# Optimization experiments

Hardware: AMD Instinct MI355X
Metric: run time of the kernel (lower is better)

Reference implementation:

```python
import jax, jax.numpy as jnp
import numpy as np

N, E, IN, H = 50000, 800000, 128, 64
BN_EPS = 1e-5


def _bn(x, g, b, m, v):
    return (x - m) * jax.lax.rsqrt(v + BN_EPS) * g + b


def _gat(x, src, dst, W, a_s, a_d, bias):
    # PyG GATConv (heads=1): project, per-edge attention with self-loops,
    # segment softmax over destination, scatter-weighted aggregation.
    h = x @ W                                  # [N, H]
    as_n = h @ a_s                             # [N]
    ad_n = h @ a_d                             # [N]
    e = jax.nn.leaky_relu(as_n[src] + ad_n[dst], 0.2)   # [E+N]
    emax = jax.ops.segment_max(e, dst, num_segments=N)
    ex = jnp.exp(e - emax[dst])
    denom = jax.ops.segment_sum(ex, dst, num_segments=N)
    alpha = ex / (denom[dst] + 1e-16)
    out = jax.ops.segment_sum(alpha[:, None] * h[src], dst, num_segments=N)
    return out + bias


def setup_inputs() -> dict:
    key = jax.random.key(0)
    ks = jax.random.split(key, 24)
    inp = {}
    inp['x'] = jax.random.normal(ks[0], (N, IN), dtype=jnp.float32)
    inp['edge_index'] = jax.random.randint(ks[1], (2, E), 0, N, dtype=jnp.int32)
    s = 0.1
    inp['conv1_W'] = jax.random.normal(ks[2], (IN, H)) * s
    inp['conv1_as'] = jax.random.normal(ks[3], (H,)) * s
    inp['conv1_ad'] = jax.random.normal(ks[4], (H,)) * s
    inp['conv1_b'] = jnp.zeros((H,))
    inp['convW'] = jax.random.normal(ks[5], (4, H, H)) * s
    inp['conv_as'] = jax.random.normal(ks[6], (4, H)) * s
    inp['conv_ad'] = jax.random.normal(ks[7], (4, H)) * s
    inp['conv_b'] = jnp.zeros((4, H))
    inp['bn_g'] = jnp.ones((5, H))
    inp['bn_b'] = jnp.zeros((5, H))
    inp['bn_m'] = jax.random.normal(ks[8], (5, H)) * 0.01
    inp['bn_v'] = jnp.ones((5, H))
    inp['projW'] = jax.random.normal(ks[9], (4, H, H)) * s
    inp['projb'] = jnp.zeros((4, H))
    inp['hW1'] = jax.random.normal(ks[10], (H, H // 2)) * s
    inp['hb1'] = jnp.zeros((H // 2,))
    inp['hbn_g'] = jnp.ones((H // 2,))
    inp['hbn_b'] = jnp.zeros((H // 2,))
    inp['hbn_m'] = jax.random.normal(ks[11], (H // 2,)) * 0.01
    inp['hbn_v'] = jnp.ones((H // 2,))
    inp['hW2'] = jax.random.normal(ks[12], (H // 2, 1)) * s
    inp['hb2'] = jnp.zeros((1,))
    return inp


def reference(x, edge_index, conv1_W, conv1_as, conv1_ad, conv1_b, convW, conv_as, conv_ad, conv_b, bn_g, bn_b, bn_m, bn_v, projW, projb, hW1, hb1, hbn_g, hbn_b, hbn_m, hbn_v, hW2, hb2):
    loop = jnp.arange(N, dtype=edge_index.dtype)
    src = jnp.concatenate([edge_index[0], loop])  # self-loops (PyG default)
    dst = jnp.concatenate([edge_index[1], loop])

    x1 = jax.nn.relu(_gat(x, src, dst, conv1_W, conv1_as, conv1_ad, conv1_b))
    x1 = _bn(x1, bn_g[0], bn_b[0], bn_m[0], bn_v[0])

    xp = x1
    for l in range(4):  # conv2..conv5 (dropout identity in eval)
        xc = jax.nn.relu(_gat(xp, src, dst, convW[l], conv_as[l], conv_ad[l], conv_b[l]))
        xc = _bn(xc, bn_g[l + 1], bn_b[l + 1], bn_m[l + 1], bn_v[l + 1]) + (xp @ projW[l] + projb[l])
        xp = xc

    g = jnp.mean(xp, axis=0, keepdims=True)      # global_mean_pool, single graph -> [1, H]
    h1 = jax.nn.relu(g @ hW1 + hb1)
    h1 = _bn(h1, hbn_g, hbn_b, hbn_m, hbn_v)
    out = (h1 @ hW2 + hb2).squeeze(-1)           # [1]
    return out
```

## Files before the change

kernel.cpp:

```cpp
#include <hip/hip_runtime.h>
#include <hip/hip_fp16.h>

#define N_NODES 50000
#define N_EDGES 800000
#define IN_F 128
#define H_F 64
#define BN_EPS 1e-5f
#define MAXDEG 48
#define POOL_NB 256

__device__ inline unsigned pkh2(float a, float b) {
    __half2 t = __floats2half2_rn(a, b);
    return *(unsigned*)&t;
}
__device__ inline float2 uph2(unsigned u) {
    __half2 t = *(__half2*)&u;
    return __half22float2(t);
}


__global__ void k_init(int* __restrict__ cnt, unsigned short* __restrict__ ssrc) {
    int i = blockIdx.x * 256 + threadIdx.x;
    if (i < N_NODES) { cnt[i] = 1; ssrc[(size_t)i * MAXDEG] = (unsigned short)i; }
}

__global__ void k_scatter(const int* __restrict__ src, const int* __restrict__ dst,
                          int* __restrict__ cnt, unsigned short* __restrict__ ssrc) {
    int i = blockIdx.x * 256 + threadIdx.x;
    int e = i * 4;
    if (e + 3 < N_EDGES) {
        int4 s4 = *(const int4*)(src + e);
        int4 d4 = *(const int4*)(dst + e);
        int p0 = atomicAdd(&cnt[d4.x], 1);
        if (p0 < MAXDEG) ssrc[(size_t)d4.x * MAXDEG + p0] = (unsigned short)s4.x;
        int p1 = atomicAdd(&cnt[d4.y], 1);
        if (p1 < MAXDEG) ssrc[(size_t)d4.y * MAXDEG + p1] = (unsigned short)s4.y;
        int p2 = atomicAdd(&cnt[d4.z], 1);
        if (p2 < MAXDEG) ssrc[(size_t)d4.z * MAXDEG + p2] = (unsigned short)s4.z;
        int p3 = atomicAdd(&cnt[d4.w], 1);
        if (p3 < MAXDEG) ssrc[(size_t)d4.w * MAXDEG + p3] = (unsigned short)s4.w;
    } else {
        for (int k = e; k < N_EDGES; k++) {
            int s = src[k], d = dst[k];
            int p = atomicAdd(&cnt[d], 1);
            if (p < MAXDEG) ssrc[(size_t)d * MAXDEG + p] = (unsigned short)s;
        }
    }
}

__global__ __launch_bounds__(256) void k_gemm1(
        const float* __restrict__ x, const float* __restrict__ W,
        const float* __restrict__ a_s, const float* __restrict__ a_d,
        __half* __restrict__ hh, float* __restrict__ asn, float* __restrict__ adn) {
    __shared__ float Xs[64 * 129];
    __shared__ float asb[4][64], adb[4][64];
    int t = threadIdx.x, lane = t & 63, wave = t >> 6;
    int row0 = blockIdx.x * 64;
    for (int i = t; i < 64 * IN_F; i += 256) {
        int r = i >> 7, c = i & 127;
        Xs[r * 129 + c] = (row0 + r < N_NODES) ? x[(size_t)(row0 + r) * IN_F + c] : 0.f;
    }
    __syncthreads();
    int jb = __builtin_amdgcn_readfirstlane(wave << 4);
    float acc[16];
    #pragma unroll
    for (int j = 0; j < 16; j++) acc[j] = 0.f;
    for (int k0 = 0; k0 < IN_F; k0 += 8) {
        float xr[8];
        #pragma unroll
        for (int kk = 0; kk < 8; kk++) xr[kk] = Xs[lane * 129 + k0 + kk];
        #pragma unroll
        for (int kk = 0; kk < 8; kk++) {
            const float* wr = W + (k0 + kk) * H_F + jb;
            #pragma unroll
            for (int j = 0; j < 16; j++) acc[j] = fmaf(xr[kk], wr[j], acc[j]);
        }
    }
    int row = row0 + lane;
    float pa = 0.f, pd = 0.f;
    #pragma unroll
    for (int j = 0; j < 16; j++) { pa += acc[j] * a_s[jb + j]; pd += acc[j] * a_d[jb + j]; }
    asb[wave][lane] = pa; adb[wave][lane] = pd;
    if (row < N_NODES) {
        uint4 w0, w1;
        w0.x = pkh2(acc[0],  acc[1]);  w0.y = pkh2(acc[2],  acc[3]);
        w0.z = pkh2(acc[4],  acc[5]);  w0.w = pkh2(acc[6],  acc[7]);
        w1.x = pkh2(acc[8],  acc[9]);  w1.y = pkh2(acc[10], acc[11]);
        w1.z = pkh2(acc[12], acc[13]); w1.w = pkh2(acc[14], acc[15]);
        uint4* hp = (uint4*)(hh + (size_t)row * H_F + jb);
        hp[0] = w0; hp[1] = w1;
    }
    __syncthreads();
    if (wave == 0 && row < N_NODES) {
        asn[row] = asb[0][lane] + asb[1][lane] + asb[2][lane] + asb[3][lane];
        adn[row] = adb[0][lane] + adb[1][lane] + adb[2][lane] + adb[3][lane];
    }
}

__global__ __launch_bounds__(256) void k_gemm(
        const float* __restrict__ xp, const float* __restrict__ W,
        const float* __restrict__ PW, const float* __restrict__ pbias,
        const float* __restrict__ a_s, const float* __restrict__ a_d,
        __half* __restrict__ hh, float* __restrict__ p,
        float* __restrict__ asn, float* __restrict__ adn) {
    __shared__ float Xs[64 * 65];
    __shared__ float asb[4][64], adb[4][64];
    int t = threadIdx.x, lane = t & 63, wave = t >> 6;
    int row0 = blockIdx.x * 64;
    for (int i = t; i < 64 * H_F; i += 256) {
        int r = i >> 6, c = i & 63;
        Xs[r * 65 + c] = (row0 + r < N_NODES) ? xp[(size_t)(row0 + r) * H_F + c] : 0.f;
    }
    __syncthreads();
    int jb = __builtin_amdgcn_readfirstlane(wave << 4);
    float acc[16], pac[16];
    #pragma unroll
    for (int j = 0; j < 16; j++) { acc[j] = 0.f; pac[j] = 0.f; }
    for (int k0 = 0; k0 < H_F; k0 += 8) {
        float xr[8];
        #pragma unroll
        for (int kk = 0; kk < 8; kk++) xr[kk] = Xs[lane * 65 + k0 + kk];
        #pragma unroll
        for (int kk = 0; kk < 8; kk++) {
            const float* wr = W  + (k0 + kk) * H_F + jb;
            const float* pr = PW + (k0 + kk) * H_F + jb;
            #pragma unroll
            for (int j = 0; j < 16; j++) {
                acc[j] = fmaf(xr[kk], wr[j], acc[j]);
                pac[j] = fmaf(xr[kk], pr[j], pac[j]);
            }
        }
    }
    int row = row0 + lane;
    float pa = 0.f, pd = 0.f;
    #pragma unroll
    for (int j = 0; j < 16; j++) { pa += acc[j] * a_s[jb + j]; pd += acc[j] * a_d[jb + j]; }
    asb[wave][lane] = pa; adb[wave][lane] = pd;
    if (row < N_NODES) {
        uint4 w0, w1;
        w0.x = pkh2(acc[0],  acc[1]);  w0.y = pkh2(acc[2],  acc[3]);
        w0.z = pkh2(acc[4],  acc[5]);  w0.w = pkh2(acc[6],  acc[7]);
        w1.x = pkh2(acc[8],  acc[9]);  w1.y = pkh2(acc[10], acc[11]);
        w1.z = pkh2(acc[12], acc[13]); w1.w = pkh2(acc[14], acc[15]);
        uint4* hp = (uint4*)(hh + (size_t)row * H_F + jb);
        hp[0] = w0; hp[1] = w1;
        float4* pp = (float4*)(p + (size_t)row * H_F + jb);
        #pragma unroll
        for (int q = 0; q < 4; q++)
            pp[q] = make_float4(pac[4*q] + pbias[jb+4*q],   pac[4*q+1] + pbias[jb+4*q+1],
                                pac[4*q+2] + pbias[jb+4*q+2], pac[4*q+3] + pbias[jb+4*q+3]);
    }
    __syncthreads();
    if (wave == 0 && row < N_NODES) {
        asn[row] = asb[0][lane] + asb[1][lane] + asb[2][lane] + asb[3][lane];
        adn[row] = adb[0][lane] + adb[1][lane] + adb[2][lane] + adb[3][lane];
    }
}

template <bool HAS_RES>
__global__ __launch_bounds__(256) void k_attn_aggr(
        const __half* __restrict__ hh, const float* __restrict__ asn, const float* __restrict__ adn,
        const int* __restrict__ cnt, const unsigned short* __restrict__ ssrc,
        const float* __restrict__ bias,
        const float* __restrict__ bg, const float* __restrict__ bb,
        const float* __restrict__ bm, const float* __restrict__ bv,
        const float* __restrict__ res, float* __restrict__ out) {
    __shared__ float          wls[4][MAXDEG];
    __shared__ unsigned short sls[4][MAXDEG];
    int t = threadIdx.x, lane = t & 63, wave = t >> 6;
    int d = blockIdx.x * 4 + wave;
    int du = __builtin_amdgcn_readfirstlane(d);
    int cn = __builtin_amdgcn_readfirstlane(cnt[du]);
    cn = cn < MAXDEG ? cn : MAXDEG;
    const unsigned short* sp = ssrc + (size_t)du * MAXDEG;
    float add = adn[du];

    float w_l = 0.f;
    if (lane < cn) {
        int s = sp[lane];
        float ev = asn[s] + add;
        ev = ev < 0.f ? 0.2f * ev : ev;
        w_l = __expf(ev);
        sls[wave][lane] = (unsigned short)s;
        wls[wave][lane] = w_l;
    }
    float ssum = w_l;
    #pragma unroll
    for (int dlt = 32; dlt > 0; dlt >>= 1) ssum += __shfl_xor(ssum, dlt);
    __syncthreads();

    int grp = lane >> 3, fl = lane & 7;
    int   se[6];
    float we[6];
    #pragma unroll
    for (int i = 0; i < 6; i++) {
        int e = grp + 8 * i;
        bool v = e < cn;
        int ec = v ? e : 0;
        se[i] = sls[wave][ec];
        we[i] = v ? wls[wave][ec] : 0.f;
    }
    uint4 r[6];
    #pragma unroll
    for (int i = 0; i < 6; i++)
        r[i] = ((const uint4*)(hh + (size_t)se[i] * H_F))[fl];
    float acc[8];
    #pragma unroll
    for (int q = 0; q < 8; q++) acc[q] = 0.f;
    #pragma unroll
    for (int i = 0; i < 6; i++) {
        float w = we[i];
        float2 f01 = uph2(r[i].x), f23 = uph2(r[i].y), f45 = uph2(r[i].z), f67 = uph2(r[i].w);
        acc[0] = fmaf(w, f01.x, acc[0]); acc[1] = fmaf(w, f01.y, acc[1]);
        acc[2] = fmaf(w, f23.x, acc[2]); acc[3] = fmaf(w, f23.y, acc[3]);
        acc[4] = fmaf(w, f45.x, acc[4]); acc[5] = fmaf(w, f45.y, acc[5]);
        acc[6] = fmaf(w, f67.x, acc[6]); acc[7] = fmaf(w, f67.y, acc[7]);
    }
    #pragma unroll
    for (int dlt = 8; dlt < 64; dlt <<= 1) {
        #pragma unroll
        for (int q = 0; q < 8; q++) acc[q] += __shfl_xor(acc[q], dlt);
    }
    if (lane < 8) {
        float inv = 1.f / (ssum + 1e-16f);
        int f0 = lane * 8;
        #pragma unroll
        for (int q = 0; q < 2; q++) {
            float4 b4 = ((const float4*)(bias + f0))[q];
            float4 g4 = ((const float4*)(bg + f0))[q];
            float4 o4 = ((const float4*)(bb + f0))[q];
            float4 m4 = ((const float4*)(bm + f0))[q];
            float4 v4 = ((const float4*)(bv + f0))[q];
            float4 o;
            o.x = fmaxf(fmaf(acc[4*q+0], inv, b4.x), 0.f);
            o.y = fmaxf(fmaf(acc[4*q+1], inv, b4.y), 0.f);
            o.z = fmaxf(fmaf(acc[4*q+2], inv, b4.z), 0.f);
            o.w = fmaxf(fmaf(acc[4*q+3], inv, b4.w), 0.f);
            o.x = (o.x - m4.x) * rsqrtf(v4.x + BN_EPS) * g4.x + o4.x;
            o.y = (o.y - m4.y) * rsqrtf(v4.y + BN_EPS) * g4.y + o4.y;
            o.z = (o.z - m4.z) * rsqrtf(v4.z + BN_EPS) * g4.z + o4.z;
            o.w = (o.w - m4.w) * rsqrtf(v4.w + BN_EPS) * g4.w + o4.w;
            if (HAS_RES) {
                float4 rr = ((const float4*)(res + (size_t)d * H_F + f0))[q];
                o.x += rr.x; o.y += rr.y; o.z += rr.z; o.w += rr.w;
            }
            ((float4*)(out + (size_t)d * H_F + f0))[q] = o;
        }
    }
}

__global__ __launch_bounds__(256) void k_pool(const float* __restrict__ x,
                                              float* __restrict__ partials) {
    __shared__ float red[256 * 4];
    int t = threadIdx.x, b = blockIdx.x;
    const float4* xv = (const float4*)x;
    const int total = N_NODES * (H_F / 4);
    float a0 = 0.f, a1 = 0.f, a2 = 0.f, a3 = 0.f;
    for (int i = b * 256 + t; i < total; i += POOL_NB * 256) {
        float4 v = xv[i];
        a0 += v.x; a1 += v.y; a2 += v.z; a3 += v.w;
    }
    red[t * 4 + 0] = a0; red[t * 4 + 1] = a1; red[t * 4 + 2] = a2; red[t * 4 + 3] = a3;
    __syncthreads();
    if (t < 64) {
        int p = t >> 2, q = t & 3;
        float s = 0.f;
        #pragma unroll
        for (int k = 0; k < 16; k++) s += red[(p + 16 * k) * 4 + q];
        partials[b * H_F + t] = s;
    }
}

__global__ __launch_bounds__(256) void k_head(
        const float* __restrict__ partials,
        const float* __restrict__ hW1, const float* __restrict__ hb1,
        const float* __restrict__ hg, const float* __restrict__ hb,
        const float* __restrict__ hm, const float* __restrict__ hv,
        const float* __restrict__ hW2, const float* __restrict__ hb2,
        float* __restrict__ out) {
    __shared__ float red[256];
    __shared__ float gl[64];
    __shared__ float h1[32];
    int t = threadIdx.x;
    int f = t & 63, g = t >> 6;
    float s = 0.f;
    for (int k = g; k < POOL_NB; k += 4) s += partials[k * H_F + f];
    red[t] = s;
    __syncthreads();
    if (t < 64) gl[t] = (red[t] + red[64 + t] + red[128 + t] + red[192 + t]) * (1.f / N_NODES);
    __syncthreads();
    if (t < 32) {
        float v = hb1[t];
        for (int l = 0; l < 64; l++) v += gl[l] * hW1[l * 32 + t];
        v = fmaxf(v, 0.f);
        v = (v - hm[t]) * rsqrtf(hv[t] + BN_EPS) * hg[t] + hb[t];
        h1[t] = v;
    }
    __syncthreads();
    if (t == 0) {
        float v = hb2[0];
        for (int j = 0; j < 32; j++) v += h1[j] * hW2[j];
        out[0] = v;
    }
}


extern "C" void kernel_launch(void* const* d_in, const int* in_sizes, int n_in,
                              void* d_out, int out_size, void* d_ws, size_t ws_size,
                              hipStream_t stream) {
    (void)in_sizes; (void)n_in; (void)out_size; (void)ws_size;
    const float* x        = (const float*)d_in[0];
    const int*   ei       = (const int*)d_in[1];
    const float* conv1_W  = (const float*)d_in[2];
    const float* conv1_as = (const float*)d_in[3];
    const float* conv1_ad = (const float*)d_in[4];
    const float* conv1_b  = (const float*)d_in[5];
    const float* convW    = (const float*)d_in[6];
    const float* conv_as  = (const float*)d_in[7];
    const float* conv_ad  = (const float*)d_in[8];
    const float* conv_b   = (const float*)d_in[9];
    const float* bn_g     = (const float*)d_in[10];
    const float* bn_b     = (const float*)d_in[11];
    const float* bn_m     = (const float*)d_in[12];
    const float* bn_v     = (const float*)d_in[13];
    const float* projW    = (const float*)d_in[14];
    const float* projb    = (const float*)d_in[15];
    const float* hW1      = (const float*)d_in[16];
    const float* hb1      = (const float*)d_in[17];
    const float* hbn_g    = (const float*)d_in[18];
    const float* hbn_b    = (const float*)d_in[19];
    const float* hbn_m    = (const float*)d_in[20];
    const float* hbn_v    = (const float*)d_in[21];
    const float* hW2      = (const float*)d_in[22];
    const float* hb2      = (const float*)d_in[23];

    const int* e_src = ei;
    const int* e_dst = ei + N_EDGES;

    char* wsb = (char*)d_ws;
    size_t cur = 0;
    auto alloc = [&](size_t bytes) -> void* {
        void* p = wsb + cur;
        cur = (cur + bytes + 255) & ~(size_t)255;
        return p;
    };
    int*            cnt      = (int*)alloc(N_NODES * sizeof(int));
    unsigned short* ssrc     = (unsigned short*)alloc((size_t)N_NODES * MAXDEG * sizeof(unsigned short));
    __half*         hh       = (__half*)alloc((size_t)N_NODES * H_F * sizeof(__half));
    float*          p        = (float*)alloc((size_t)N_NODES * H_F * sizeof(float));
    float*          asn      = (float*)alloc(N_NODES * sizeof(float));
    float*          adn      = (float*)alloc(N_NODES * sizeof(float));
    float*          xa       = (float*)alloc((size_t)N_NODES * H_F * sizeof(float));
    float*          xb       = (float*)alloc((size_t)N_NODES * H_F * sizeof(float));
    float*          partials = (float*)alloc(POOL_NB * H_F * sizeof(float));

    dim3 blk(256);

    k_init<<<dim3((N_NODES + 255) / 256), blk, 0, stream>>>(cnt, ssrc);
    k_scatter<<<dim3((N_EDGES / 4 + 255) / 256), blk, 0, stream>>>(e_src, e_dst, cnt, ssrc);

    dim3 gemm_grid((N_NODES + 63) / 64);
    dim3 aggr_grid((N_NODES + 3) / 4);

    k_gemm1<<<gemm_grid, blk, 0, stream>>>(x, conv1_W, conv1_as, conv1_ad, hh, asn, adn);
    k_attn_aggr<false><<<aggr_grid, blk, 0, stream>>>(hh, asn, adn, cnt, ssrc, conv1_b,
                                                      bn_g, bn_b, bn_m, bn_v, nullptr, xa);

    float* bufs[2] = { xa, xb };
    for (int l = 0; l < 4; l++) {
        float* in  = bufs[l & 1];
        float* out = bufs[(l + 1) & 1];
        k_gemm<<<gemm_grid, blk, 0, stream>>>(in, convW + (size_t)l * H_F * H_F,
                                              projW + (size_t)l * H_F * H_F, projb + l * H_F,
                                              conv_as + l * H_F, conv_ad + l * H_F,
                                              hh, p, asn, adn);
        k_attn_aggr<true><<<aggr_grid, blk, 0, stream>>>(hh, asn, adn, cnt, ssrc,
                                                         conv_b + l * H_F,
                                                         bn_g + (l + 1) * H_F, bn_b + (l + 1) * H_F,
                                                         bn_m + (l + 1) * H_F, bn_v + (l + 1) * H_F,
                                                         p, out);
    }

    k_pool<<<dim3(POOL_NB), blk, 0, stream>>>(xa, partials);
    k_head<<<dim3(1), blk, 0, stream>>>(partials, hW1, hb1, hbn_g, hbn_b, hbn_m, hbn_v,
                                        hW2, hb2, (float*)d_out);
}
```

Baseline: 476.4 us.

## Split feature table into two halves and run aggregation per half for cache fit

The fp16 projected-feature table is stored as two separate 32-column arrays, and the attention aggregation kernel is launched twice per layer, once per half, each gathering only 32 features per source. Each gathered half-table is about 3.2 MB, which lets the random neighbour gathers hit in L2/LLC more often than the full table does. The cost is that attention weights, softmax and adjacency reads are recomputed twice and there are extra kernel launches. The edge scatter is also split into two launches and loses its scalar tail path.

```diff
diff --git a/kernel.cpp b/kernel.cpp
--- a/kernel.cpp
+++ b/kernel.cpp
@@ -5,9 +5,12 @@
 #define N_EDGES 800000
 #define IN_F 128
 #define H_F 64
+#define HALF_F 32
 #define BN_EPS 1e-5f
 #define MAXDEG 48
 #define POOL_NB 256
+#define NQUAD (N_EDGES / 4)
+#define QHALF (NQUAD / 2)
 
 __device__ inline unsigned pkh2(float a, float b) {
     __half2 t = __floats2half2_rn(a, b);
@@ -25,33 +28,28 @@
 }
 
 __global__ void k_scatter(const int* __restrict__ src, const int* __restrict__ dst,
-                          int* __restrict__ cnt, unsigned short* __restrict__ ssrc) {
-    int i = blockIdx.x * 256 + threadIdx.x;
-    int e = i * 4;
-    if (e + 3 < N_EDGES) {
-        int4 s4 = *(const int4*)(src + e);
-        int4 d4 = *(const int4*)(dst + e);
-        int p0 = atomicAdd(&cnt[d4.x], 1);
-        if (p0 < MAXDEG) ssrc[(size_t)d4.x * MAXDEG + p0] = (unsigned short)s4.x;
-        int p1 = atomicAdd(&cnt[d4.y], 1);
-        if (p1 < MAXDEG) ssrc[(size_t)d4.y * MAXDEG + p1] = (unsigned short)s4.y;
-        int p2 = atomicAdd(&cnt[d4.z], 1);
-        if (p2 < MAXDEG) ssrc[(size_t)d4.z * MAXDEG + p2] = (unsigned short)s4.z;
-        int p3 = atomicAdd(&cnt[d4.w], 1);
-        if (p3 < MAXDEG) ssrc[(size_t)d4.w * MAXDEG + p3] = (unsigned short)s4.w;
-    } else {
-        for (int k = e; k < N_EDGES; k++) {
-            int s = src[k], d = dst[k];
-            int p = atomicAdd(&cnt[d], 1);
-            if (p < MAXDEG) ssrc[(size_t)d * MAXDEG + p] = (unsigned short)s;
-        }
-    }
+                          int* __restrict__ cnt, unsigned short* __restrict__ ssrc,
+                          int qbase, int qend) {
+    int q = qbase + blockIdx.x * 256 + threadIdx.x;
+    if (q >= qend) return;
+    int e = q * 4;
+    int4 s4 = *(const int4*)(src + e);
+    int4 d4 = *(const int4*)(dst + e);
+    int p0 = atomicAdd(&cnt[d4.x], 1);
+    if (p0 < MAXDEG) ssrc[(size_t)d4.x * MAXDEG + p0] = (unsigned short)s4.x;
+    int p1 = atomicAdd(&cnt[d4.y], 1);
+    if (p1 < MAXDEG) ssrc[(size_t)d4.y * MAXDEG + p1] = (unsigned short)s4.y;
+    int p2 = atomicAdd(&cnt[d4.z], 1);
+    if (p2 < MAXDEG) ssrc[(size_t)d4.z * MAXDEG + p2] = (unsigned short)s4.z;
+    int p3 = atomicAdd(&cnt[d4.w], 1);
+    if (p3 < MAXDEG) ssrc[(size_t)d4.w * MAXDEG + p3] = (unsigned short)s4.w;
 }
 
 __global__ __launch_bounds__(256) void k_gemm1(
         const float* __restrict__ x, const float* __restrict__ W,
         const float* __restrict__ a_s, const float* __restrict__ a_d,
-        __half* __restrict__ hh, float* __restrict__ asn, float* __restrict__ adn) {
+        __half* __restrict__ hh_lo, __half* __restrict__ hh_hi,
+        float* __restrict__ asn, float* __restrict__ adn) {
     __shared__ float Xs[64 * 129];
     __shared__ float asb[4][64], adb[4][64];
     int t = threadIdx.x, lane = t & 63, wave = t >> 6;
@@ -87,7 +85,9 @@
         w0.z = pkh2(acc[4],  acc[5]);  w0.w = pkh2(acc[6],  acc[7]);
         w1.x = pkh2(acc[8],  acc[9]);  w1.y = pkh2(acc[10], acc[11]);
         w1.z = pkh2(acc[12], acc[13]); w1.w = pkh2(acc[14], acc[15]);
-        uint4* hp = (uint4*)(hh + (size_t)row * H_F + jb);
+        __half* dstb = (jb < HALF_F) ? (hh_lo + (size_t)row * HALF_F + jb)
+                                     : (hh_hi + (size_t)row * HALF_F + (jb - HALF_F));
+        uint4* hp = (uint4*)dstb;
         hp[0] = w0; hp[1] = w1;
     }
     __syncthreads();
@@ -101,7 +101,8 @@
         const float* __restrict__ xp, const float* __restrict__ W,
         const float* __restrict__ PW, const float* __restrict__ pbias,
         const float* __restrict__ a_s, const float* __restrict__ a_d,
-        __half* __restrict__ hh, float* __restrict__ p,
+        __half* __restrict__ hh_lo, __half* __restrict__ hh_hi,
+        float* __restrict__ p,
         float* __restrict__ asn, float* __restrict__ adn) {
     __shared__ float Xs[64 * 65];
     __shared__ float asb[4][64], adb[4][64];
@@ -142,7 +143,9 @@
         w0.z = pkh2(acc[4],  acc[5]);  w0.w = pkh2(acc[6],  acc[7]);
         w1.x = pkh2(acc[8],  acc[9]);  w1.y = pkh2(acc[10], acc[11]);
         w1.z = pkh2(acc[12], acc[13]); w1.w = pkh2(acc[14], acc[15]);
-        uint4* hp = (uint4*)(hh + (size_t)row * H_F + jb);
+        __half* dstb = (jb < HALF_F) ? (hh_lo + (size_t)row * HALF_F + jb)
+                                     : (hh_hi + (size_t)row * HALF_F + (jb - HALF_F));
+        uint4* hp = (uint4*)dstb;
         hp[0] = w0; hp[1] = w1;
         float4* pp = (float4*)(p + (size_t)row * H_F + jb);
         #pragma unroll
@@ -157,9 +160,9 @@
     }
 }
 
-template <bool HAS_RES>
+template <bool HAS_RES, int HALF>
 __global__ __launch_bounds__(256) void k_attn_aggr(
-        const __half* __restrict__ hh, const float* __restrict__ asn, const float* __restrict__ adn,
+        const __half* __restrict__ hhH, const float* __restrict__ asn, const float* __restrict__ adn,
         const int* __restrict__ cnt, const unsigned short* __restrict__ ssrc,
         const float* __restrict__ bias,
         const float* __restrict__ bg, const float* __restrict__ bb,
@@ -200,52 +203,47 @@
         se[i] = sls[wave][ec];
         we[i] = v ? wls[wave][ec] : 0.f;
     }
-    uint4 r[6];
+    uint2 r[6];
     #pragma unroll
     for (int i = 0; i < 6; i++)
-        r[i] = ((const uint4*)(hh + (size_t)se[i] * H_F))[fl];
-    float acc[8];
-    #pragma unroll
-    for (int q = 0; q < 8; q++) acc[q] = 0.f;
+        r[i] = ((const uint2*)(hhH + (size_t)se[i] * HALF_F))[fl];
+    float acc[4];
+    #pragma unroll
+    for (int q = 0; q < 4; q++) acc[q] = 0.f;
     #pragma unroll
     for (int i = 0; i < 6; i++) {
         float w = we[i];
-        float2 f01 = uph2(r[i].x), f23 = uph2(r[i].y), f45 = uph2(r[i].z), f67 = uph2(r[i].w);
+        float2 f01 = uph2(r[i].x), f23 = uph2(r[i].y);
         acc[0] = fmaf(w, f01.x, acc[0]); acc[1] = fmaf(w, f01.y, acc[1]);
         acc[2] = fmaf(w, f23.x, acc[2]); acc[3] = fmaf(w, f23.y, acc[3]);
-        acc[4] = fmaf(w, f45.x, acc[4]); acc[5] = fmaf(w, f45.y, acc[5]);
-        acc[6] = fmaf(w, f67.x, acc[6]); acc[7] = fmaf(w, f67.y, acc[7]);
     }
     #pragma unroll
     for (int dlt = 8; dlt < 64; dlt <<= 1) {
         #pragma unroll
-        for (int q = 0; q < 8; q++) acc[q] += __shfl_xor(acc[q], dlt);
+        for (int q = 0; q < 4; q++) acc[q] += __shfl_xor(acc[q], dlt);
     }
     if (lane < 8) {
         float inv = 1.f / (ssum + 1e-16f);
-        int f0 = lane * 8;
-        #pragma unroll
-        for (int q = 0; q < 2; q++) {
-            float4 b4 = ((const float4*)(bias + f0))[q];
-            float4 g4 = ((const float4*)(bg + f0))[q];
-            float4 o4 = ((const float4*)(bb + f0))[q];
-            float4 m4 = ((const float4*)(bm + f0))[q];
-            float4 v4 = ((const float4*)(bv + f0))[q];
-            float4 o;
-            o.x = fmaxf(fmaf(acc[4*q+0], inv, b4.x), 0.f);
-            o.y = fmaxf(fmaf(acc[4*q+1], inv, b4.y), 0.f);
-            o.z = fmaxf(fmaf(acc[4*q+2], inv, b4.z), 0.f);
-            o.w = fmaxf(fmaf(acc[4*q+3], inv, b4.w), 0.f);
-            o.x = (o.x - m4.x) * rsqrtf(v4.x + BN_EPS) * g4.x + o4.x;
-            o.y = (o.y - m4.y) * rsqrtf(v4.y + BN_EPS) * g4.y + o4.y;
-            o.z = (o.z - m4.z) * rsqrtf(v4.z + BN_EPS) * g4.z + o4.z;
-            o.w = (o.w - m4.w) * rsqrtf(v4.w + BN_EPS) * g4.w + o4.w;
-            if (HAS_RES) {
-                float4 rr = ((const float4*)(res + (size_t)d * H_F + f0))[q];
-                o.x += rr.x; o.y += rr.y; o.z += rr.z; o.w += rr.w;
-            }
-            ((float4*)(out + (size_t)d * H_F + f0))[q] = o;
+        int fg = HALF * HALF_F + lane * 4;
+        float4 b4 = *(const float4*)(bias + fg);
+        float4 g4 = *(const float4*)(bg + fg);
+        float4 o4 = *(const float4*)(bb + fg);
+        float4 m4 = *(const float4*)(bm + fg);
+        float4 v4 = *(const float4*)(bv + fg);
+        float4 o;
+        o.x = fmaxf(fmaf(acc[0], inv, b4.x), 0.f);
+        o.y = fmaxf(fmaf(acc[1], inv, b4.y), 0.f);
+        o.z = fmaxf(fmaf(acc[2], inv, b4.z), 0.f);
+        o.w = fmaxf(fmaf(acc[3], inv, b4.w), 0.f);
+        o.x = (o.x - m4.x) * rsqrtf(v4.x + BN_EPS) * g4.x + o4.x;
+        o.y = (o.y - m4.y) * rsqrtf(v4.y + BN_EPS) * g4.y + o4.y;
+        o.z = (o.z - m4.z) * rsqrtf(v4.z + BN_EPS) * g4.z + o4.z;
+        o.w = (o.w - m4.w) * rsqrtf(v4.w + BN_EPS) * g4.w + o4.w;
+        if (HAS_RES) {
+            float4 rr = *(const float4*)(res + (size_t)d * H_F + fg);
+            o.x += rr.x; o.y += rr.y; o.z += rr.z; o.w += rr.w;
         }
+        *(float4*)(out + (size_t)d * H_F + fg) = o;
     }
 }
 
@@ -346,7 +344,8 @@
     };
     int*            cnt      = (int*)alloc(N_NODES * sizeof(int));
     unsigned short* ssrc     = (unsigned short*)alloc((size_t)N_NODES * MAXDEG * sizeof(unsigned short));
-    __half*         hh       = (__half*)alloc((size_t)N_NODES * H_F * sizeof(__half));
+    __half*         hh_lo    = (__half*)alloc((size_t)N_NODES * HALF_F * sizeof(__half));
+    __half*         hh_hi    = (__half*)alloc((size_t)N_NODES * HALF_F * sizeof(__half));
     float*          p        = (float*)alloc((size_t)N_NODES * H_F * sizeof(float));
     float*          asn      = (float*)alloc(N_NODES * sizeof(float));
     float*          adn      = (float*)alloc(N_NODES * sizeof(float));
@@ -357,14 +356,17 @@
     dim3 blk(256);
 
     k_init<<<dim3((N_NODES + 255) / 256), blk, 0, stream>>>(cnt, ssrc);
-    k_scatter<<<dim3((N_EDGES / 4 + 255) / 256), blk, 0, stream>>>(e_src, e_dst, cnt, ssrc);
+    k_scatter<<<dim3((QHALF + 255) / 256), blk, 0, stream>>>(e_src, e_dst, cnt, ssrc, 0, QHALF);
+    k_scatter<<<dim3((QHALF + 255) / 256), blk, 0, stream>>>(e_src, e_dst, cnt, ssrc, QHALF, NQUAD);
 
     dim3 gemm_grid((N_NODES + 63) / 64);
-    dim3 aggr_grid((N_NODES + 3) / 4);
-
-    k_gemm1<<<gemm_grid, blk, 0, stream>>>(x, conv1_W, conv1_as, conv1_ad, hh, asn, adn);
-    k_attn_aggr<false><<<aggr_grid, blk, 0, stream>>>(hh, asn, adn, cnt, ssrc, conv1_b,
-                                                      bn_g, bn_b, bn_m, bn_v, nullptr, xa);
+    dim3 aggr_grid(N_NODES / 4);
+
+    k_gemm1<<<gemm_grid, blk, 0, stream>>>(x, conv1_W, conv1_as, conv1_ad, hh_lo, hh_hi, asn, adn);
+    k_attn_aggr<false, 0><<<aggr_grid, blk, 0, stream>>>(hh_lo, asn, adn, cnt, ssrc, conv1_b,
+                                                         bn_g, bn_b, bn_m, bn_v, nullptr, xa);
+    k_attn_aggr<false, 1><<<aggr_grid, blk, 0, stream>>>(hh_hi, asn, adn, cnt, ssrc, conv1_b,
+                                                         bn_g, bn_b, bn_m, bn_v, nullptr, xa);
 
     float* bufs[2] = { xa, xb };
     for (int l = 0; l < 4; l++) {
@@ -373,12 +375,17 @@
         k_gemm<<<gemm_grid, blk, 0, stream>>>(in, convW + (size_t)l * H_F * H_F,
                                               projW + (size_t)l * H_F * H_F, projb + l * H_F,
                                               conv_as + l * H_F, conv_ad + l * H_F,
-                                              hh, p, asn, adn);
-        k_attn_aggr<true><<<aggr_grid, blk, 0, stream>>>(hh, asn, adn, cnt, ssrc,
-                                                         conv_b + l * H_F,
-                                                         bn_g + (l + 1) * H_F, bn_b + (l + 1) * H_F,
-                                                         bn_m + (l + 1) * H_F, bn_v + (l + 1) * H_F,
-                                                         p, out);
+                                              hh_lo, hh_hi, p, asn, adn);
+        k_attn_aggr<true, 0><<<aggr_grid, blk, 0, stream>>>(hh_lo, asn, adn, cnt, ssrc,
+                                                            conv_b + l * H_F,
+                                                            bn_g + (l + 1) * H_F, bn_b + (l + 1) * H_F,
+                                                            bn_m + (l + 1) * H_F, bn_v + (l + 1) * H_F,
+                                                            p, out);
+        k_attn_aggr<true, 1><<<aggr_grid, blk, 0, stream>>>(hh_hi, asn, adn, cnt, ssrc,
+                                                            conv_b + l * H_F,
+                                                            bn_g + (l + 1) * H_F, bn_b + (l + 1) * H_F,
+                                                            bn_m + (l + 1) * H_F, bn_v + (l + 1) * H_F,
+                                                            p, out);
     }
 
     k_pool<<<dim3(POOL_NB), blk, 0, stream>>>(xa, partials);
```

Result: slower. 556.9 us (+16.9%).
